# Optimization experiments

Hardware: AMD Instinct MI355X
Metric: run time of the kernel (lower is better)

The kernel has to match this reference:

```python
import jax, jax.numpy as jnp
import numpy as np

BS, SL, NN, NE = 8, 100, 200, 600
C = 110; CP1 = C + 1
D = 128          # node_embed_dim
DC = 64          # concept_embed_dim
H = 256          # lstm hidden
VOCAB = 50000
NPROB = 1000
FEAT = 2 + CP1 + DC  # LSTM input dim = 177


def setup_inputs() -> dict:
    key = jax.random.key(0)
    ks = jax.random.split(key, 24)
    f32 = jnp.float32
    p_id = jax.random.randint(ks[0], (BS, SL), 0, NPROB)
    c_id = jax.random.bernoulli(ks[1], 0.1, (BS, SL, CP1)).astype(f32)
    node_id = jax.random.randint(ks[2], (BS, SL, NN), 0, VOCAB)
    edge = jax.random.randint(ks[3], (BS, SL, 2, NE), 0, NN)
    edge_type = jax.random.randint(ks[4], (BS, SL, NE), 0, 8)
    target_c = jax.random.bernoulli(ks[5], 0.05, (BS, SL, CP1)).astype(f32)
    target_c = target_c.at[:, :, 0].set(1.0)  # every step has >=1 target concept
    result = jax.random.bernoulli(ks[6], 0.5, (BS * SL, 1)).astype(f32)
    c_embed = jax.random.bernoulli(ks[7], 0.1, (BS, SL, CP1)).astype(f32)
    cur_result = jax.random.normal(ks[8], (BS, SL, 2), f32)
    # parameters
    node_embed_w = jax.random.normal(ks[9], (VOCAB, D), f32) * 0.02
    edge_embed_w = (jax.random.normal(ks[10], (8, D), f32) * 0.02).at[0].set(0.0)  # padding_idx=0
    ggnn_w = jax.random.normal(ks[11], (4, D, D), f32) * 0.05
    gru_w_ih = jax.random.normal(ks[12], (3 * D, D), f32) * 0.05
    gru_w_hh = jax.random.normal(ks[13], (3 * D, D), f32) * 0.05
    gru_b_ih = jnp.zeros((3 * D,), f32)
    gru_b_hh = jnp.zeros((3 * D,), f32)
    transdim_w = jax.random.normal(ks[14], (DC, D), f32) * 0.05
    concept_embedding = jax.random.normal(ks[15], (CP1, DC), f32) * 0.05
    lstm_w_ih = jax.random.normal(ks[16], (4 * H, FEAT), f32) * 0.05
    lstm_w_hh = jax.random.normal(ks[17], (4 * H, H), f32) * 0.05
    lstm_b_ih = jnp.zeros((4 * H,), f32)
    lstm_b_hh = jnp.zeros((4 * H,), f32)
    pred_w = jax.random.normal(ks[18], (CP1, H), f32) * 0.05
    pred_b = jnp.zeros((CP1,), f32)
    return dict(p_id=p_id, c_id=c_id, node_id=node_id, edge=edge, edge_type=edge_type,
                target_c=target_c, result=result, c_embed=c_embed, cur_result=cur_result,
                node_embed_w=node_embed_w, edge_embed_w=edge_embed_w, ggnn_w=ggnn_w,
                gru_w_ih=gru_w_ih, gru_w_hh=gru_w_hh, gru_b_ih=gru_b_ih, gru_b_hh=gru_b_hh,
                transdim_w=transdim_w, concept_embedding=concept_embedding,
                lstm_w_ih=lstm_w_ih, lstm_w_hh=lstm_w_hh, lstm_b_ih=lstm_b_ih,
                lstm_b_hh=lstm_b_hh, pred_w=pred_w, pred_b=pred_b)


def _forward(p_id, c_id, node_id, edge, edge_type, target_c, result, c_embed, cur_result,
             node_embed_w, edge_embed_w, ggnn_w, gru_w_ih, gru_w_hh, gru_b_ih, gru_b_hh,
             transdim_w, concept_embedding, lstm_w_ih, lstm_w_hh, lstm_b_ih, lstm_b_hh,
             pred_w, pred_b):
    bs, sl = p_id.shape
    N = node_id.shape[2]
    G = bs * sl  # all graphs batched (replaces torch per-sample python loop)
    x = node_embed_w[node_id].reshape(G, N, -1)                       # [G,N,D]
    ew = edge_embed_w[edge_type].mean(-1).reshape(G, -1, 1)           # [G,E,1]
    e = edge.reshape(G, 2, -1)
    src, dst = e[:, 0], e[:, 1]                                       # [G,E]
    flat_dst = (dst + jnp.arange(G)[:, None] * N).reshape(-1)
    d = x.shape[-1]
    # GatedGraphConv, 4 layers: m = x @ W_l, sum-aggregate edge_weight*m[src] at dst, GRUCell update
    for l in range(4):
        m = jnp.einsum('gnd,de->gne', x, ggnn_w[l])
        gathered = jnp.take_along_axis(m, src[:, :, None], axis=1)    # [G,E,D]
        msg = (ew * gathered).reshape(-1, d)
        agg = jax.ops.segment_sum(msg, flat_dst, num_segments=G * N).reshape(G, N, d)
        gi = agg @ gru_w_ih.T + gru_b_ih
        gh = x @ gru_w_hh.T + gru_b_hh
        i_r, i_z, i_n = jnp.split(gi, 3, axis=-1)
        h_r, h_z, h_n = jnp.split(gh, 3, axis=-1)
        r = jax.nn.sigmoid(i_r + h_r)
        z = jax.nn.sigmoid(i_z + h_z)
        n = jnp.tanh(i_n + r * h_n)
        x = (1.0 - z) * n + z * x
    # transdim (node_embed_dim != concept_embed_dim)
    ggnn = jnp.einsum('gnd,cd->gnc', x, transdim_w)                   # [G,N,DC]
    # concept-node attention
    ce = c_embed.reshape(G, -1, 1)                                    # [G,C+1,1]
    query = ce * concept_embedding[None]                              # [G,C+1,DC]
    attn_w = jax.nn.softmax(jnp.einsum('gcd,gnd->gcn', query, ggnn), axis=2)
    attn = jnp.einsum('gcn,gnd->gcd', attn_w, ggnn) * ce
    num = jnp.sum(c_id, axis=2).reshape(G, 1)
    num = jnp.where(num == 0, 1.0, num)
    attn_out = (jnp.sum(attn, axis=1) / num).reshape(bs, sl, -1)
    # LSTM (1 layer, batch_first)
    lstm_in = jnp.concatenate([c_embed, attn_out, cur_result], axis=2)
    hdim = pred_w.shape[1]
    def step(carry, xt):
        h, c = carry
        gates = xt @ lstm_w_ih.T + lstm_b_ih + h @ lstm_w_hh.T + lstm_b_hh
        i, f, g, o = jnp.split(gates, 4, axis=-1)
        c = jax.nn.sigmoid(f) * c + jax.nn.sigmoid(i) * jnp.tanh(g)
        h = jax.nn.sigmoid(o) * jnp.tanh(c)
        return (h, c), h
    init = (jnp.zeros((bs, hdim), lstm_in.dtype), jnp.zeros((bs, hdim), lstm_in.dtype))
    _, hs = jax.lax.scan(step, init, jnp.swapaxes(lstm_in, 0, 1))
    lstm_out = jnp.swapaxes(hs, 0, 1).reshape(G, hdim)
    # prediction + masked BCE-with-logits
    pred = lstm_out @ pred_w.T + pred_b                               # [G,C+1]
    tc = target_c.reshape(G, -1)
    pred1 = jnp.sum(pred * tc, axis=1)
    nc = jnp.sum(tc, axis=1)
    mask = nc > 0
    fp = pred1 / jnp.where(mask, nc, 1.0)
    ft = result.reshape(-1)
    bce = jnp.maximum(fp, 0.0) - fp * ft + jnp.log1p(jnp.exp(-jnp.abs(fp)))
    mf = mask.astype(fp.dtype)
    loss = jnp.sum(bce * mf) / jnp.maximum(jnp.sum(mf), 1.0)
    return loss, jax.nn.sigmoid(fp), ft


def reference(p_id, c_id, node_id, edge, edge_type, target_c, result, c_embed, cur_result,
              node_embed_w, edge_embed_w, ggnn_w, gru_w_ih, gru_w_hh, gru_b_ih, gru_b_hh,
              transdim_w, concept_embedding, lstm_w_ih, lstm_w_hh, lstm_b_ih, lstm_b_hh,
              pred_w, pred_b):
    return _forward(p_id, c_id, node_id, edge, edge_type, target_c, result, c_embed, cur_result,
                    node_embed_w, edge_embed_w, ggnn_w, gru_w_ih, gru_w_hh, gru_b_ih, gru_b_hh,
                    transdim_w, concept_embedding, lstm_w_ih, lstm_w_hh, lstm_b_ih, lstm_b_hh,
                    pred_w, pred_b)
```

## Files before the change

### kernel.cpp

```cpp
#include <hip/hip_runtime.h>
#include <math.h>

static const int BSZ   = 8;
static const int SLN   = 100;
static const int NNODE = 200;
static const int NEDGE = 600;
static const int CP1N  = 111;
static const int DIM   = 128;
static const int DCN   = 64;
static const int HID   = 256;
static const int FEATN = 177;
static const int GN    = 800;
static const int MROW  = 160000;

typedef unsigned short u16;
typedef u16    u16x8  __attribute__((ext_vector_type(8)));
typedef __bf16 bf16x8 __attribute__((ext_vector_type(8)));
typedef __bf16 bf16x2 __attribute__((ext_vector_type(2)));
typedef float  f32x16 __attribute__((ext_vector_type(16)));

#if defined(__has_builtin)
# if __has_builtin(__builtin_amdgcn_fdot2_f32_bf16)
#  define HAVE_FDOT2 1
# else
#  define HAVE_FDOT2 0
# endif
#else
# define HAVE_FDOT2 0
#endif

__device__ __forceinline__ float sigf(float v){ return 1.0f/(1.0f + expf(-v)); }
__device__ __forceinline__ u16 f2bf(float f){
    union { float f; unsigned u; } v; v.f = f;
    unsigned r = v.u + 0x7FFFu + ((v.u >> 16) & 1u);
    return (u16)(r >> 16);
}
__device__ __forceinline__ float bf2f(u16 u){
    union { unsigned u; float f; } v; v.u = ((unsigned)u) << 16;
    return v.f;
}
__device__ __forceinline__ float dot2bf(unsigned w, unsigned h, float acc){
#if HAVE_FDOT2
    return __builtin_amdgcn_fdot2_f32_bf16(__builtin_bit_cast(bf16x2, w),
                                           __builtin_bit_cast(bf16x2, h), acc, false);
#else
    acc += bf2f((u16)(w & 0xffffu)) * bf2f((u16)(h & 0xffffu));
    acc += bf2f((u16)(w >> 16))     * bf2f((u16)(h >> 16));
    return acc;
#endif
}

__global__ void k_transpose_w(const float* __restrict__ whh, const float* __restrict__ wih,
                              unsigned* __restrict__ whhP, float* __restrict__ wihT){
    int idx = blockIdx.x*blockDim.x + threadIdx.x;
    const int total1 = 128*1024;
    if (idx < total1){
        int k2 = idx >> 10, p = idx & 1023;
        int jq = (p & 3)*256 + (p >> 2);
        u16 lo = f2bf(whh[(size_t)jq*256 + 2*k2]);
        u16 hi = f2bf(whh[(size_t)jq*256 + 2*k2 + 1]);
        whhP[(size_t)k2*1024 + p] = (unsigned)lo | ((unsigned)hi << 16);
    }
    int idx2 = idx - total1;
    const int total2 = FEATN*1024;
    if (idx2 >= 0 && idx2 < total2){
        int k = idx2 >> 10, j = idx2 & 1023;
        wihT[(size_t)k*1024 + j] = wih[(size_t)j*FEATN + k];
    }
}

__global__ void k_convert_w(const float* __restrict__ wih, const float* __restrict__ whh,
                            const float* __restrict__ gw, const float* __restrict__ tw,
                            u16* __restrict__ wihb, u16* __restrict__ whhb,
                            u16* __restrict__ gwTb, u16* __restrict__ twb){
    int idx = blockIdx.x*blockDim.x + threadIdx.x;
    if (idx < 49152){
        wihb[idx] = f2bf(wih[idx]);
    } else if (idx < 98304){
        int t = idx - 49152;
        whhb[t] = f2bf(whh[t]);
    } else if (idx < 163840){
        int t = idx - 98304;
        int l = t >> 14, rem = t & 16383, n = rem >> 7, k = rem & 127;
        gwTb[t] = f2bf(gw[((size_t)l*128 + k)*128 + n]);
    } else if (idx < 172032){
        int t = idx - 163840;
        twb[t] = f2bf(tw[t]);
    }
}

__global__ void __launch_bounds__(256)
k_build_csr(const int* __restrict__ edge, const int* __restrict__ etype,
            const float* __restrict__ eembed,
            int* __restrict__ csr_src, float* __restrict__ csr_w, int* __restrict__ csr_off){
    int g = blockIdx.x; int tid = threadIdx.x;
    __shared__ float tmean[8];
    __shared__ float tpart[8][32];
    __shared__ int cnt[NNODE];
    __shared__ int offs[NNODE+1];
    __shared__ int cur[NNODE];
    {
        int ty = tid >> 5, lane = tid & 31;
        float s = 0.f;
        for (int i = lane; i < DIM; i += 32) s += eembed[ty*DIM + i];
        tpart[ty][lane] = s;
    }
    for (int i = tid; i < NNODE; i += 256) cnt[i] = 0;
    __syncthreads();
    if (tid < 8){
        float s = 0.f;
        for (int i = 0; i < 32; i++) s += tpart[tid][i];
        tmean[tid] = s / (float)DIM;
    }
    for (int e = tid; e < NEDGE; e += 256){
        int dst = edge[((size_t)g*2+1)*NEDGE + e];
        atomicAdd(&cnt[dst], 1);
    }
    __syncthreads();
    if (tid == 0){
        int run = 0;
        for (int i = 0; i < NNODE; i++){ offs[i] = run; run += cnt[i]; }
        offs[NNODE] = run;
    }
    __syncthreads();
    for (int i = tid; i < NNODE; i += 256) cur[i] = offs[i];
    for (int i = tid; i < NNODE+1; i += 256) csr_off[(size_t)g*(NNODE+1)+i] = offs[i];
    __syncthreads();
    for (int e = tid; e < NEDGE; e += 256){
        int dst = edge[((size_t)g*2+1)*NEDGE + e];
        int src = edge[((size_t)g*2+0)*NEDGE + e];
        float w = tmean[etype[(size_t)g*NEDGE + e]];
        int pos = atomicAdd(&cur[dst], 1);
        csr_src[(size_t)g*NEDGE + pos] = src;
        csr_w [(size_t)g*NEDGE + pos] = w;
    }
}

__global__ void k_gather_x(const int* __restrict__ nid, const float4* __restrict__ emb,
                           u16x8* __restrict__ xb){
    const long total = (long)MROW*16;
    for (long c = (long)blockIdx.x*blockDim.x + threadIdx.x; c < total; c += (long)gridDim.x*blockDim.x){
        long row = c >> 4; int p = (int)(c & 15);
        float4 a = emb[(size_t)nid[row]*32 + p*2];
        float4 b = emb[(size_t)nid[row]*32 + p*2 + 1];
        u16x8 v;
        v[0]=f2bf(a.x); v[1]=f2bf(a.y); v[2]=f2bf(a.z); v[3]=f2bf(a.w);
        v[4]=f2bf(b.x); v[5]=f2bf(b.y); v[6]=f2bf(b.z); v[7]=f2bf(b.w);
        xb[c] = v;
    }
}

__global__ void __launch_bounds__(256)
k_mm_scatter(const u16* __restrict__ xb, const u16* __restrict__ gwTb_l,
             const int* __restrict__ csr_src, const float* __restrict__ csr_w,
             const int* __restrict__ csr_off, u16* __restrict__ aggb){
    __shared__ u16 smem[224*128];
    __shared__ int   e_src[NEDGE];
    __shared__ float e_w[NEDGE];
    __shared__ int   offs_s[NNODE+1];
    int g = blockIdx.x;
    int tid = threadIdx.x;
    const u16x8* xg = (const u16x8*)(xb + (size_t)g*NNODE*DIM);
    u16x8* afrag = (u16x8*)smem;
    for (int c = tid; c < 3584; c += 256){
        int row = c >> 4, kc8 = c & 15;
        u16x8 v = {};
        if (row < NNODE) v = xg[row*16 + kc8];
        afrag[((row>>5)*8 + (kc8>>1))*64 + (row&31) + 32*(kc8&1)] = v;
    }
    {
        const int*   srcp = csr_src + (size_t)g*NEDGE;
        const float* wp   = csr_w   + (size_t)g*NEDGE;
        const int*   off  = csr_off + (size_t)g*(NNODE+1);
        for (int i = tid; i < NEDGE; i += 256){ e_src[i] = srcp[i]; e_w[i] = wp[i]; }
        for (int i = tid; i <= NNODE; i += 256) offs_s[i] = off[i];
    }
    __syncthreads();
    int w = tid >> 6, lane = tid & 63;
    int nbase = w*32;
    int m = lane & 31, kh = lane >> 5;
    f32x16 acc[7];
    #pragma unroll
    for (int t = 0; t < 7; t++) acc[t] = (f32x16)0.f;
    const u16x8* bp = (const u16x8*)gwTb_l;
    int nrow = nbase + m;
    #pragma unroll
    for (int kc = 0; kc < 8; kc++){
        u16x8 b = bp[nrow*16 + kc*2 + kh];
        #pragma unroll
        for (int mt = 0; mt < 7; mt++){
            u16x8 a = afrag[(mt*8 + kc)*64 + lane];
            acc[mt] = __builtin_amdgcn_mfma_f32_32x32x16_bf16(
                __builtin_bit_cast(bf16x8, a), __builtin_bit_cast(bf16x8, b), acc[mt], 0, 0, 0);
        }
    }
    __syncthreads();
    #pragma unroll
    for (int mt = 0; mt < 7; mt++){
        #pragma unroll
        for (int r = 0; r < 16; r++){
            int row = mt*32 + (r&3) + 8*(r>>2) + 4*kh;
            int col = nbase + m;
            smem[row*128 + col] = f2bf(acc[mt][r]);
        }
    }
    __syncthreads();
    const unsigned* m32 = (const unsigned*)smem;
    int j2 = tid & 63, rg = tid >> 6;
    unsigned* aggout = (unsigned*)(aggb + (size_t)g*NNODE*DIM);
    for (int i = 0; i < 50; i++){
        int n = rg*50 + i;
        int b0 = offs_s[n], e0 = offs_s[n+1];
        float a0 = 0.f, a1 = 0.f;
        for (int p = b0; p < e0; p++){
            unsigned mv = m32[e_src[p]*64 + j2];
            float w_ = e_w[p];
            a0 += w_ * bf2f((u16)(mv & 0xffffu));
            a1 += w_ * bf2f((u16)(mv >> 16));
        }
        aggout[(size_t)n*64 + j2] = (unsigned)f2bf(a0) | ((unsigned)f2bf(a1) << 16);
    }
}

__global__ void __launch_bounds__(512, 2)
k_gru_mfma(u16* __restrict__ xb, const u16* __restrict__ aggb,
           const u16* __restrict__ wihb, const u16* __restrict__ whhb,
           const float* __restrict__ bih, const float* __restrict__ bhh){
    __shared__ u16x8 afragA[2048];
    __shared__ u16x8 afragX[2048];
    int tid = threadIdx.x;
    long r0 = (long)blockIdx.x * 128;
    const u16x8* aggp = (const u16x8*)aggb;
    const u16x8* xbp  = (const u16x8*)xb;
    for (int c = tid; c < 4096; c += 512){
        int mat = c >> 11, cc = c & 2047;
        int row = cc >> 4, kc8 = cc & 15;
        u16x8 v = (mat ? xbp : aggp)[(r0 + row)*16 + kc8];
        int slot = ((row>>5)*8 + (kc8>>1))*64 + (row&31) + 32*(kc8&1);
        (mat ? afragX : afragA)[slot] = v;
    }
    __syncthreads();
    int w = tid >> 6, lane = tid & 63;
    int mtg = w >> 2;
    int cb  = (w & 3) * 32;
    f32x16 acc0[6], acc1[6];
    #pragma unroll
    for (int t = 0; t < 6; t++){ acc0[t] = (f32x16)0.f; acc1[t] = (f32x16)0.f; }
    const u16x8* bi = (const u16x8*)wihb;
    const u16x8* bh = (const u16x8*)whhb;
    int kh = lane >> 5;
    int ncol = cb + (lane & 31);
    #pragma unroll
    for (int kc = 0; kc < 8; kc++){
        u16x8 aA0 = afragA[((2*mtg+0)*8 + kc)*64 + lane];
        u16x8 aA1 = afragA[((2*mtg+1)*8 + kc)*64 + lane];
        u16x8 aX0 = afragX[((2*mtg+0)*8 + kc)*64 + lane];
        u16x8 aX1 = afragX[((2*mtg+1)*8 + kc)*64 + lane];
        #pragma unroll
        for (int g3 = 0; g3 < 3; g3++){
            int n = g3*128 + ncol;
            u16x8 b1 = bi[n*16 + kc*2 + kh];
            u16x8 b2 = bh[n*16 + kc*2 + kh];
            acc0[g3]   = __builtin_amdgcn_mfma_f32_32x32x16_bf16(
                __builtin_bit_cast(bf16x8, aA0), __builtin_bit_cast(bf16x8, b1), acc0[g3], 0,0,0);
            acc1[g3]   = __builtin_amdgcn_mfma_f32_32x32x16_bf16(
                __builtin_bit_cast(bf16x8, aA1), __builtin_bit_cast(bf16x8, b1), acc1[g3], 0,0,0);
            acc0[3+g3] = __builtin_amdgcn_mfma_f32_32x32x16_bf16(
                __builtin_bit_cast(bf16x8, aX0), __builtin_bit_cast(bf16x8, b2), acc0[3+g3], 0,0,0);
            acc1[3+g3] = __builtin_amdgcn_mfma_f32_32x32x16_bf16(
                __builtin_bit_cast(bf16x8, aX1), __builtin_bit_cast(bf16x8, b2), acc1[3+g3], 0,0,0);
        }
    }
    int col = cb + (lane & 31);
    float bir = bih[col], biz = bih[col+128], bin = bih[col+256];
    float bhr = bhh[col], bhz = bhh[col+128], bhn = bhh[col+256];
    int kc8c = col >> 3, elc = col & 7;
    #pragma unroll
    for (int mt2 = 0; mt2 < 2; mt2++){
        const f32x16* ac = mt2 ? acc1 : acc0;
        #pragma unroll
        for (int r = 0; r < 16; r++){
            int row = mtg*64 + mt2*32 + (r&3) + 8*(r>>2) + 4*kh;
            u16x8 xv = afragX[((row>>5)*8 + (kc8c>>1))*64 + (row&31) + 32*(kc8c&1)];
            float xo = bf2f(((const u16*)&xv)[elc]);
            float rr  = sigf(ac[0][r] + bir + ac[3][r] + bhr);
            float zz  = sigf(ac[1][r] + biz + ac[4][r] + bhz);
            float nn_ = tanhf(ac[2][r] + bin + rr*(ac[5][r] + bhn));
            float xn  = (1.f - zz)*nn_ + zz*xo;
            xb[(size_t)(r0 + row)*DIM + col] = f2bf(xn);
        }
    }
}

__global__ void __launch_bounds__(256)
k_transdim(const u16* __restrict__ xb, const u16* __restrict__ twb, u16* __restrict__ out){
    int tid = threadIdx.x;
    int w = tid >> 6, lane = tid & 63;
    int m = lane & 31, kh = lane >> 5;
    long r0 = (long)blockIdx.x * 128;
    const u16x8* xp = (const u16x8*)xb;
    const u16x8* tp = (const u16x8*)twb;
    long rowA = r0 + w*32 + m;
    f32x16 acc[2];
    acc[0] = (f32x16)0.f; acc[1] = (f32x16)0.f;
    #pragma unroll
    for (int kc = 0; kc < 8; kc++){
        u16x8 a = xp[rowA*16 + kc*2 + kh];
        #pragma unroll
        for (int nt = 0; nt < 2; nt++){
            u16x8 b = tp[(nt*32 + m)*16 + kc*2 + kh];
            acc[nt] = __builtin_amdgcn_mfma_f32_32x32x16_bf16(
                __builtin_bit_cast(bf16x8, a), __builtin_bit_cast(bf16x8, b), acc[nt], 0,0,0);
        }
    }
    #pragma unroll
    for (int nt = 0; nt < 2; nt++){
        #pragma unroll
        for (int r = 0; r < 16; r++){
            int row = w*32 + (r&3) + 8*(r>>2) + 4*kh;
            int col = nt*32 + m;
            out[(r0 + row)*DCN + col] = f2bf(acc[nt][r]);
        }
    }
}

__global__ void __launch_bounds__(256)
k_attention(const u16* __restrict__ gout, const float* __restrict__ cemb,
            const float* __restrict__ cid, const float* __restrict__ conc,
            const float* __restrict__ curres, float* __restrict__ lstm_in){
    int g = blockIdx.x; int tid = threadIdx.x;
    int lane = tid & 63, wv = tid >> 6;
    __shared__ float gg[NNODE*65];
    __shared__ float ce_s[CP1N];
    __shared__ float sc[256];
    __shared__ float wredA[4];
    __shared__ float wredB[4];
    __shared__ float part[4][DCN];
    __shared__ float oacc[DCN];
    __shared__ float num_s;
    if (tid < CP1N) ce_s[tid] = cemb[(size_t)g*CP1N + tid];
    if (tid < DCN) oacc[tid] = 0.f;
    for (int i = tid; i < NNODE*DCN; i += 256){
        int n = i >> 6, d = i & 63;
        gg[n*65 + d] = bf2f(gout[(size_t)g*NNODE*DCN + i]);
    }
    {
        float v = (tid < CP1N) ? cid[(size_t)g*CP1N + tid] : 0.f;
        #pragma unroll
        for (int m2 = 32; m2; m2 >>= 1) v += __shfl_xor(v, m2);
        if (lane == 0) wredA[wv] = v;
    }
    __syncthreads();
    if (tid == 0){
        float nm = wredA[0]+wredA[1]+wredA[2]+wredA[3];
        num_s = (nm == 0.f) ? 1.f : nm;
    }
    __syncthreads();
    for (int c = 0; c < CP1N; c++){
        float ce = ce_s[c];
        if (ce == 0.f) continue;
        const float* qc = conc + c*DCN;
        float s = -1e30f;
        if (tid < NNODE){
            float a_ = 0.f;
            const float* gr_ = &gg[tid*65];
            #pragma unroll 16
            for (int d = 0; d < DCN; d++) a_ += qc[d] * gr_[d];
            s = ce * a_;
        }
        float m_ = s;
        #pragma unroll
        for (int m2 = 32; m2; m2 >>= 1) m_ = fmaxf(m_, __shfl_xor(m_, m2));
        if (lane == 0) wredA[wv] = m_;
        __syncthreads();
        float mx = fmaxf(fmaxf(wredA[0], wredA[1]), fmaxf(wredA[2], wredA[3]));
        float e = (tid < NNODE) ? expf(s - mx) : 0.f;
        sc[tid] = e;
        float sum_ = e;
        #pragma unroll
        for (int m2 = 32; m2; m2 >>= 1) sum_ += __shfl_xor(sum_, m2);
        if (lane == 0) wredB[wv] = sum_;
        __syncthreads();
        float inv = ce / (wredB[0]+wredB[1]+wredB[2]+wredB[3]);
        float pa = 0.f;
        for (int n = wv; n < NNODE; n += 4) pa += sc[n] * gg[n*65 + lane];
        part[wv][lane] = pa;
        __syncthreads();
        if (tid < DCN) oacc[tid] += inv * (part[0][tid] + part[1][tid] + part[2][tid] + part[3][tid]);
    }
    __syncthreads();
    if (tid < FEATN){
        float v;
        if      (tid < CP1N)       v = ce_s[tid];
        else if (tid < CP1N+DCN)   v = oacc[tid-CP1N] / num_s;
        else                       v = curres[(size_t)g*2 + (tid-CP1N-DCN)];
        lstm_in[(size_t)g*FEATN + tid] = v;
    }
}

__global__ void __launch_bounds__(256)
k_gi(const float* __restrict__ lstm_in, const float* __restrict__ wihT,
     const float* __restrict__ bih, const float* __restrict__ bhh, float* __restrict__ gi){
    int rb = blockIdx.x;
    int jb = blockIdx.y;
    int tid = threadIdx.x;
    __shared__ float in_s[8][FEATN];
    for (int i = tid; i < 8*FEATN; i += 256){ int r = i/FEATN, k = i%FEATN; in_s[r][k] = lstm_in[((size_t)rb*8+r)*FEATN + k]; }
    __syncthreads();
    int j = jb*256 + tid;
    float acc[8];
    #pragma unroll
    for (int i = 0; i < 8; i++) acc[i] = 0.f;
    for (int k = 0; k < FEATN; k++){
        float w = wihT[(size_t)k*1024 + j];
        #pragma unroll
        for (int i = 0; i < 8; i++) acc[i] += in_s[i][k] * w;
    }
    float b = bih[j] + bhh[j];
    int jp = (j & 255)*4 + (j >> 8);
    #pragma unroll
    for (int i = 0; i < 8; i++) gi[((size_t)rb*8+i)*1024 + jp] = acc[i] + b;
}

static const int WREG = 104;
static const int WL4  = 6;

__global__ void __launch_bounds__(1024)
__attribute__((amdgpu_waves_per_eu(4,4)))
k_lstm(const float* __restrict__ gi, const unsigned* __restrict__ whhP, float* __restrict__ out){
    int b = blockIdx.x; int tid = threadIdx.x;
    __shared__ uint4 ldsw4[WL4][1024];
    __shared__ unsigned hbuf[2][128];
    unsigned wreg[WREG];
    #pragma unroll
    for (int i = 0; i < WREG; i++) wreg[i] = whhP[(size_t)i*1024 + tid];
    #pragma unroll
    for (int q = 0; q < WL4; q++){
        uint4 v;
        v.x = whhP[(size_t)(WREG + 4*q + 0)*1024 + tid];
        v.y = whhP[(size_t)(WREG + 4*q + 1)*1024 + tid];
        v.z = whhP[(size_t)(WREG + 4*q + 2)*1024 + tid];
        v.w = whhP[(size_t)(WREG + 4*q + 3)*1024 + tid];
        ldsw4[q][tid] = v;
    }
    if (tid < 128) hbuf[0][tid] = 0u;
    float c_reg = 0.f;
    int lane = tid & 63;
    int hq = tid >> 2;
    __syncthreads();
    unsigned hv0 = hbuf[0][lane];
    unsigned hv1 = hbuf[0][64 + lane];
    float giv = gi[(size_t)b*SLN*1024 + tid];
    for (int t = 0; t < SLN; t++){
        float acc0 = giv, acc1 = 0.f;
        if (t+1 < SLN) giv = gi[((size_t)b*SLN + t + 1)*1024 + tid];
        #pragma unroll
        for (int p = 0; p < 64; p += 2){
            unsigned hpa = (unsigned)__builtin_amdgcn_readlane((int)hv0, p);
            unsigned hpb = (unsigned)__builtin_amdgcn_readlane((int)hv0, p+1);
            acc0 = dot2bf(wreg[p],   hpa, acc0);
            acc1 = dot2bf(wreg[p+1], hpb, acc1);
        }
        #pragma unroll
        for (int p = 64; p < WREG; p += 2){
            unsigned hpa = (unsigned)__builtin_amdgcn_readlane((int)hv1, p - 64);
            unsigned hpb = (unsigned)__builtin_amdgcn_readlane((int)hv1, p - 63);
            acc0 = dot2bf(wreg[p],   hpa, acc0);
            acc1 = dot2bf(wreg[p+1], hpb, acc1);
        }
        #pragma unroll
        for (int q = 0; q < WL4; q++){
            uint4 wv = ldsw4[q][tid];
            int base = WREG + 4*q - 64;
            unsigned h0 = (unsigned)__builtin_amdgcn_readlane((int)hv1, base + 0);
            unsigned h1 = (unsigned)__builtin_amdgcn_readlane((int)hv1, base + 1);
            unsigned h2 = (unsigned)__builtin_amdgcn_readlane((int)hv1, base + 2);
            unsigned h3 = (unsigned)__builtin_amdgcn_readlane((int)hv1, base + 3);
            acc0 = dot2bf(wv.x, h0, acc0);
            acc1 = dot2bf(wv.y, h1, acc1);
            acc0 = dot2bf(wv.z, h2, acc0);
            acc1 = dot2bf(wv.w, h3, acc1);
        }
        float gval = acc0 + acc1;
        float v0 = __shfl(gval, 0, 4);
        float v1 = __shfl(gval, 1, 4);
        float v2 = __shfl(gval, 2, 4);
        float v3 = __shfl(gval, 3, 4);
        float i_ = sigf(v0);
        float f_ = sigf(v1);
        float g_ = tanhf(v2);
        float o_ = sigf(v3);
        c_reg = f_*c_reg + i_*g_;
        float h = o_*tanhf(c_reg);
        int nb = (t+1) & 1;
        if ((tid & 3) == 0){
            out[((size_t)b*SLN + t)*HID + hq] = h;
            ((u16*)hbuf[nb])[hq] = f2bf(h);
        }
        __syncthreads();
        hv0 = hbuf[nb][lane];
        hv1 = hbuf[nb][64 + lane];
    }
}

__global__ void __launch_bounds__(128)
k_final(const float* __restrict__ lstm_out, const float* __restrict__ pw, const float* __restrict__ pb,
        const float* __restrict__ tc, const float* __restrict__ result,
        float* __restrict__ out, float* __restrict__ lacc){
    int row = blockIdx.x; int tid = threadIdx.x;
    __shared__ __align__(16) float h_s[HID];
    __shared__ float redv[128], redn[128];
    h_s[tid]       = lstm_out[(size_t)row*HID + tid];
    h_s[tid + 128] = lstm_out[(size_t)row*HID + tid + 128];
    __syncthreads();
    float v = 0.f, n = 0.f;
    if (tid < CP1N){
        float acc = pb[tid];
        const float4* wr = (const float4*)(pw + (size_t)tid*HID);
        const float4* hp = (const float4*)h_s;
        #pragma unroll 8
        for (int k4 = 0; k4 < 64; k4++){
            float4 w = wr[k4]; float4 h4 = hp[k4];
            acc += h4.x*w.x + h4.y*w.y + h4.z*w.z + h4.w*w.w;
        }
        float t = tc[(size_t)row*CP1N + tid];
        v = acc*t; n = t;
    }
    redv[tid] = v; redn[tid] = n;
    __syncthreads();
    for (int s = 64; s > 0; s >>= 1){
        if (tid < s){ redv[tid] += redv[tid+s]; redn[tid] += redn[tid+s]; }
        __syncthreads();
    }
    if (tid == 0){
        float nc = redn[0];
        bool mask = nc > 0.f;
        float fp = redv[0] / (mask ? nc : 1.f);
        float ft = result[row];
        float bce = fmaxf(fp, 0.f) - fp*ft + log1pf(expf(-fabsf(fp)));
        out[1 + row]      = 1.f/(1.f + expf(-fp));
        out[1 + GN + row] = ft;
        if (mask){ atomicAdd(&lacc[0], bce); atomicAdd(&lacc[1], 1.f); }
    }
}

__global__ void k_loss_final(const float* __restrict__ lacc, float* __restrict__ out){
    out[0] = lacc[0] / fmaxf(lacc[1], 1.f);
}

extern "C" void kernel_launch(void* const* d_in, const int* in_sizes, int n_in,
                              void* d_out, int out_size, void* d_ws, size_t ws_size,
                              hipStream_t stream) {
    const float* c_id        = (const float*)d_in[1];
    const int*   node_id     = (const int*)  d_in[2];
    const int*   edge        = (const int*)  d_in[3];
    const int*   etype       = (const int*)  d_in[4];
    const float* target_c    = (const float*)d_in[5];
    const float* result      = (const float*)d_in[6];
    const float* c_embed     = (const float*)d_in[7];
    const float* cur_result  = (const float*)d_in[8];
    const float* node_emb_w  = (const float*)d_in[9];
    const float* edge_emb_w  = (const float*)d_in[10];
    const float* ggnn_w      = (const float*)d_in[11];
    const float* gru_w_ih    = (const float*)d_in[12];
    const float* gru_w_hh    = (const float*)d_in[13];
    const float* gru_b_ih    = (const float*)d_in[14];
    const float* gru_b_hh    = (const float*)d_in[15];
    const float* transdim_w  = (const float*)d_in[16];
    const float* concept     = (const float*)d_in[17];
    const float* lstm_w_ih   = (const float*)d_in[18];
    const float* lstm_w_hh   = (const float*)d_in[19];
    const float* lstm_b_ih   = (const float*)d_in[20];
    const float* lstm_b_hh   = (const float*)d_in[21];
    const float* pred_w      = (const float*)d_in[22];
    const float* pred_b      = (const float*)d_in[23];
    float* out = (float*)d_out;

    char* ws = (char*)d_ws;
    size_t off = 0;
    auto alloc = [&](size_t bytes) -> void* {
        void* p = ws + off;
        off += (bytes + 255) & ~(size_t)255;
        return p;
    };
    u16*      xb       = (u16*)     alloc((size_t)MROW*DIM*2);
    u16*      aggb     = (u16*)     alloc((size_t)MROW*DIM*2);
    int*      csr_src  = (int*)     alloc((size_t)GN*NEDGE*4);
    float*    csr_w    = (float*)   alloc((size_t)GN*NEDGE*4);
    int*      csr_off  = (int*)     alloc((size_t)GN*(NNODE+1)*4);
    float*    lstm_in  = (float*)   alloc((size_t)GN*FEATN*4);
    float*    gi       = (float*)   alloc((size_t)GN*1024*4);
    unsigned* whhP     = (unsigned*)alloc((size_t)128*1024*4);
    float*    wihT     = (float*)   alloc((size_t)FEATN*1024*4);
    float*    lstm_out = (float*)   alloc((size_t)GN*HID*4);
    u16*      wihb     = (u16*)     alloc((size_t)384*128*2);
    u16*      whhb     = (u16*)     alloc((size_t)384*128*2);
    u16*      gwTb     = (u16*)     alloc((size_t)4*128*128*2);
    u16*      twb      = (u16*)     alloc((size_t)DCN*DIM*2);
    float*    lacc     = (float*)   alloc(256);
    u16*      ggnn_out = (u16*)aggb;

    hipMemsetAsync(lacc, 0, 8, stream);
    {
        int total = 128*1024 + FEATN*1024;
        k_transpose_w<<<(total + 255)/256, 256, 0, stream>>>(lstm_w_hh, lstm_w_ih, whhP, wihT);
    }
    k_convert_w<<<672, 256, 0, stream>>>(gru_w_ih, gru_w_hh, ggnn_w, transdim_w, wihb, whhb, gwTb, twb);
    k_build_csr<<<GN, 256, 0, stream>>>(edge, etype, edge_emb_w, csr_src, csr_w, csr_off);
    k_gather_x<<<4096, 256, 0, stream>>>(node_id, (const float4*)node_emb_w, (u16x8*)xb);
    for (int l = 0; l < 4; l++){
        k_mm_scatter<<<GN, 256, 0, stream>>>(xb, gwTb + (size_t)l*DIM*DIM,
                                             csr_src, csr_w, csr_off, aggb);
        k_gru_mfma<<<MROW/128, 512, 0, stream>>>(xb, aggb, wihb, whhb, gru_b_ih, gru_b_hh);
    }
    k_transdim<<<MROW/128, 256, 0, stream>>>(xb, twb, ggnn_out);
    k_attention<<<GN, 256, 0, stream>>>(ggnn_out, c_embed, c_id, concept, cur_result, lstm_in);
    k_gi<<<dim3(100, 4), 256, 0, stream>>>(lstm_in, wihT, lstm_b_ih, lstm_b_hh, gi);
    k_lstm<<<BSZ, 1024, 0, stream>>>(gi, whhP, lstm_out);
    k_final<<<GN, 128, 0, stream>>>(lstm_out, pred_w, pred_b, target_c, result, out, lacc);
    k_loss_final<<<1, 1, 0, stream>>>(lacc, out);
}
```

Measured before the change: 1.363 ms.

## Swizzle MFMA A-fragment LDS layout and restructure LSTM gate exchange via shared memory

Adds an XOR swizzle to the LDS slot layout of the A fragments in the scatter and GRU kernels, so reads and writes avoid bank conflicts. Separately, the LSTM recurrence drops the interleaved gate permutation and the 4-lane shuffle exchange. Gates now go through a shared-memory array with an extra barrier per step, and 256 threads compute the cell update. This trades shuffles for an additional __syncthreads in the serial 100-step loop and leaves 3/4 of the threads idle during the activation phase.

```diff
diff --git a/kernel.cpp b/kernel.cpp
--- a/kernel.cpp
+++ b/kernel.cpp
@@ -50,16 +50,21 @@
 #endif
 }
 
+__device__ __forceinline__ int afrag_slot(int row, int kc8){
+    int kcq = kc8 >> 1;
+    int pos = (row & 31) + 32*(kc8 & 1);
+    return ((row >> 5)*8 + kcq)*64 + (pos ^ kcq);
+}
+
 __global__ void k_transpose_w(const float* __restrict__ whh, const float* __restrict__ wih,
                               unsigned* __restrict__ whhP, float* __restrict__ wihT){
     int idx = blockIdx.x*blockDim.x + threadIdx.x;
     const int total1 = 128*1024;
     if (idx < total1){
-        int k2 = idx >> 10, p = idx & 1023;
-        int jq = (p & 3)*256 + (p >> 2);
-        u16 lo = f2bf(whh[(size_t)jq*256 + 2*k2]);
-        u16 hi = f2bf(whh[(size_t)jq*256 + 2*k2 + 1]);
-        whhP[(size_t)k2*1024 + p] = (unsigned)lo | ((unsigned)hi << 16);
+        int k2 = idx >> 10, j = idx & 1023;
+        u16 lo = f2bf(whh[(size_t)j*256 + 2*k2]);
+        u16 hi = f2bf(whh[(size_t)j*256 + 2*k2 + 1]);
+        whhP[(size_t)k2*1024 + j] = (unsigned)lo | ((unsigned)hi << 16);
     }
     int idx2 = idx - total1;
     const int total2 = FEATN*1024;
@@ -166,7 +171,7 @@
         int row = c >> 4, kc8 = c & 15;
         u16x8 v = {};
         if (row < NNODE) v = xg[row*16 + kc8];
-        afrag[((row>>5)*8 + (kc8>>1))*64 + (row&31) + 32*(kc8&1)] = v;
+        afrag[afrag_slot(row, kc8)] = v;
     }
     {
         const int*   srcp = csr_src + (size_t)g*NEDGE;
@@ -189,7 +194,7 @@
         u16x8 b = bp[nrow*16 + kc*2 + kh];
         #pragma unroll
         for (int mt = 0; mt < 7; mt++){
-            u16x8 a = afrag[(mt*8 + kc)*64 + lane];
+            u16x8 a = afrag[(mt*8 + kc)*64 + (lane ^ kc)];
             acc[mt] = __builtin_amdgcn_mfma_f32_32x32x16_bf16(
                 __builtin_bit_cast(bf16x8, a), __builtin_bit_cast(bf16x8, b), acc[mt], 0, 0, 0);
         }
@@ -236,8 +241,7 @@
         int mat = c >> 11, cc = c & 2047;
         int row = cc >> 4, kc8 = cc & 15;
         u16x8 v = (mat ? xbp : aggp)[(r0 + row)*16 + kc8];
-        int slot = ((row>>5)*8 + (kc8>>1))*64 + (row&31) + 32*(kc8&1);
-        (mat ? afragX : afragA)[slot] = v;
+        (mat ? afragX : afragA)[afrag_slot(row, kc8)] = v;
     }
     __syncthreads();
     int w = tid >> 6, lane = tid & 63;
@@ -252,10 +256,11 @@
     int ncol = cb + (lane & 31);
     #pragma unroll
     for (int kc = 0; kc < 8; kc++){
-        u16x8 aA0 = afragA[((2*mtg+0)*8 + kc)*64 + lane];
-        u16x8 aA1 = afragA[((2*mtg+1)*8 + kc)*64 + lane];
-        u16x8 aX0 = afragX[((2*mtg+0)*8 + kc)*64 + lane];
-        u16x8 aX1 = afragX[((2*mtg+1)*8 + kc)*64 + lane];
+        int lx = lane ^ kc;
+        u16x8 aA0 = afragA[((2*mtg+0)*8 + kc)*64 + lx];
+        u16x8 aA1 = afragA[((2*mtg+1)*8 + kc)*64 + lx];
+        u16x8 aX0 = afragX[((2*mtg+0)*8 + kc)*64 + lx];
+        u16x8 aX1 = afragX[((2*mtg+1)*8 + kc)*64 + lx];
         #pragma unroll
         for (int g3 = 0; g3 < 3; g3++){
             int n = g3*128 + ncol;
@@ -281,7 +286,7 @@
         #pragma unroll
         for (int r = 0; r < 16; r++){
             int row = mtg*64 + mt2*32 + (r&3) + 8*(r>>2) + 4*kh;
-            u16x8 xv = afragX[((row>>5)*8 + (kc8c>>1))*64 + (row&31) + 32*(kc8c&1)];
+            u16x8 xv = afragX[afrag_slot(row, kc8c)];
             float xo = bf2f(((const u16*)&xv)[elc]);
             float rr  = sigf(ac[0][r] + bir + ac[3][r] + bhr);
             float zz  = sigf(ac[1][r] + biz + ac[4][r] + bhz);
@@ -417,9 +422,8 @@
         for (int i = 0; i < 8; i++) acc[i] += in_s[i][k] * w;
     }
     float b = bih[j] + bhh[j];
-    int jp = (j & 255)*4 + (j >> 8);
-    #pragma unroll
-    for (int i = 0; i < 8; i++) gi[((size_t)rb*8+i)*1024 + jp] = acc[i] + b;
+    #pragma unroll
+    for (int i = 0; i < 8; i++) gi[((size_t)rb*8+i)*1024 + j] = acc[i] + b;
 }
 
 static const int WREG = 104;
@@ -430,7 +434,8 @@
 k_lstm(const float* __restrict__ gi, const unsigned* __restrict__ whhP, float* __restrict__ out){
     int b = blockIdx.x; int tid = threadIdx.x;
     __shared__ uint4 ldsw4[WL4][1024];
-    __shared__ unsigned hbuf[2][128];
+    __shared__ float gates[1024];
+    __shared__ __align__(8) u16 h16[HID];
     unsigned wreg[WREG];
     #pragma unroll
     for (int i = 0; i < WREG; i++) wreg[i] = whhP[(size_t)i*1024 + tid];
@@ -443,15 +448,14 @@
         v.w = whhP[(size_t)(WREG + 4*q + 3)*1024 + tid];
         ldsw4[q][tid] = v;
     }
-    if (tid < 128) hbuf[0][tid] = 0u;
+    if (tid < 128) ((unsigned*)h16)[tid] = 0u;
     float c_reg = 0.f;
     int lane = tid & 63;
-    int hq = tid >> 2;
-    __syncthreads();
-    unsigned hv0 = hbuf[0][lane];
-    unsigned hv1 = hbuf[0][64 + lane];
+    __syncthreads();
     float giv = gi[(size_t)b*SLN*1024 + tid];
     for (int t = 0; t < SLN; t++){
+        unsigned hv0 = ((const unsigned*)h16)[lane];
+        unsigned hv1 = ((const unsigned*)h16)[64 + lane];
         float acc0 = giv, acc1 = 0.f;
         if (t+1 < SLN) giv = gi[((size_t)b*SLN + t + 1)*1024 + tid];
         #pragma unroll
@@ -481,25 +485,19 @@
             acc0 = dot2bf(wv.z, h2, acc0);
             acc1 = dot2bf(wv.w, h3, acc1);
         }
-        float gval = acc0 + acc1;
-        float v0 = __shfl(gval, 0, 4);
-        float v1 = __shfl(gval, 1, 4);
-        float v2 = __shfl(gval, 2, 4);
-        float v3 = __shfl(gval, 3, 4);
-        float i_ = sigf(v0);
-        float f_ = sigf(v1);
-        float g_ = tanhf(v2);
-        float o_ = sigf(v3);
-        c_reg = f_*c_reg + i_*g_;
-        float h = o_*tanhf(c_reg);
-        int nb = (t+1) & 1;
-        if ((tid & 3) == 0){
-            out[((size_t)b*SLN + t)*HID + hq] = h;
-            ((u16*)hbuf[nb])[hq] = f2bf(h);
-        }
+        gates[tid] = acc0 + acc1;
         __syncthreads();
-        hv0 = hbuf[nb][lane];
-        hv1 = hbuf[nb][64 + lane];
+        if (tid < HID){
+            float i_ = sigf(gates[tid]);
+            float f_ = sigf(gates[tid+256]);
+            float g_ = tanhf(gates[tid+512]);
+            float o_ = sigf(gates[tid+768]);
+            c_reg = f_*c_reg + i_*g_;
+            float h = o_*tanhf(c_reg);
+            out[((size_t)b*SLN + t)*HID + tid] = h;
+            h16[tid] = f2bf(h);
+        }
+        __syncthreads();
     }
 }
 
```

New measurement: 1.314 ms. 3.6% less time.
